# Kernel optimization log

Measured on AMD Instinct MI355X. Metric: run time of the kernel, lower is better.

Reference implementation:

```python
import jax, jax.numpy as jnp
import numpy as np
from jax import lax

B, M, L = 4, 20, 200
IN_C, C1, C2 = 2048, 512, 256
CDIM, DC1, DC2, SDIM = 300, 512, 256, 1024
NEG = -1e15  # -INFINITY in source


def conv1d(x, w, b, pad):
    # x: [N, Cin, L], w: [Cout, Cin, K]
    y = lax.conv_general_dilated(x, w, (1,), ((pad, pad),),
                                 dimension_numbers=('NCH', 'OIH', 'NCH'))
    return y + b[None, :, None]


def maxpool2(x):
    return lax.reduce_window(x, -jnp.inf, lax.max, (1, 1, 2), (1, 1, 2), 'VALID')


def deconv1d(x, w, b):
    # torch ConvTranspose1d(k=4, s=2, p=1): conv with lhs_dilation=2, pad k-1-p=2,
    # kernel flipped and in/out swapped. w: [Cin, Cout, K]
    wt = jnp.flip(w, -1).transpose(1, 0, 2)  # [Cout, Cin, K]
    y = lax.conv_general_dilated(x, wt, (1,), ((2, 2),), lhs_dilation=(2,),
                                 dimension_numbers=('NCH', 'OIH', 'NCH'))
    return y + b[None, :, None]


def setup_inputs() -> dict:
    key = jax.random.key(0)
    ks = jax.random.split(key, 16)
    p = lambda k, sh, s=0.02: (jax.random.normal(k, sh, jnp.float32) * s)
    return dict(
        batch=jax.random.normal(ks[0], (B, M, L, IN_C), jnp.float32),
        seg_len=jax.random.randint(ks[1], (B, M), 1, L + 1, jnp.int32),
        concept1=jax.random.normal(ks[2], (B, CDIM), jnp.float32),
        concept2=jax.random.normal(ks[3], (B, CDIM), jnp.float32),
        w_conv1=p(ks[4], (C1, IN_C, 5)), b_conv1=jnp.zeros((C1,), jnp.float32),
        w_conv2=p(ks[5], (C2, C1, 5)), b_conv2=jnp.zeros((C2,), jnp.float32),
        w_ca1=p(ks[6], (C2, CDIM)), w_ca2=p(ks[7], (C2, C2)), w_ca3=p(ks[8], (1, C2)),
        w_dc1=p(ks[9], (3 * C2, DC1, 4)), b_dc1=jnp.zeros((DC1,), jnp.float32),
        w_dc2=p(ks[10], (DC1, DC2, 4)), b_dc2=jnp.zeros((DC2,), jnp.float32),
        w_sim1=p(ks[11], (SDIM, DC2)), w_sim2=p(ks[12], (SDIM, CDIM)),
        w_mlp=p(ks[13], (1, SDIM)), b_mlp=jnp.zeros((1,), jnp.float32),
    )


def reference(batch, seg_len, concept1, concept2,
              w_conv1, b_conv1, w_conv2, b_conv2,
              w_ca1, w_ca2, w_ca3,
              w_dc1, b_dc1, w_dc2, b_dc2,
              w_sim1, w_sim2, w_mlp, b_mlp):
    Bs, Ms, Ls = batch.shape[:3]
    Lq = Ls // 4
    x = batch.reshape(Bs * Ms, Ls, -1).transpose(0, 2, 1)        # [BM, IN_C, L]
    t1 = maxpool2(conv1d(x, w_conv1, b_conv1, 2))                # [BM, C1, L/2]
    t2 = maxpool2(conv1d(t1, w_conv2, b_conv2, 2)).transpose(0, 2, 1)  # [BM, L/4, C2]

    # vectorized ragged mask: k < ceil(seg_len/4)
    mask = (jnp.arange(Lq)[None, None, :] < ((seg_len + 3) // 4)[:, :, None])
    mask = mask.reshape(Bs * Ms, Lq)

    kproj = t2 @ w_ca2.T                                         # [BM, Lq, C2]

    def concept_att(concept):
        # additive attention; scores are identical across the query-frame dim,
        # so compute one row and broadcast the weighted sum.
        q = concept @ w_ca1.T                                    # [B, C2]
        qe = jnp.repeat(q, Ms, axis=0)                           # [BM, C2]
        s = jnp.tanh(qe[:, None, :] + kproj) @ w_ca3[0]          # [BM, Lq]
        s = jnp.where(mask, s, NEG)
        a = jax.nn.softmax(s, axis=-1)
        r = jnp.einsum('bk,bkc->bc', a, t2)                      # [BM, C2]
        return jnp.broadcast_to(r[:, None, :], t2.shape)         # [BM, Lq, C2]

    r1 = concept_att(concept1)
    r2 = concept_att(concept2)

    cat = jnp.concatenate([t2, r1, r2], axis=-1).transpose(0, 2, 1)  # [BM, 3C2, Lq]
    d = deconv1d(cat, w_dc1, b_dc1)                              # [BM, DC1, L/2]
    d = deconv1d(d, w_dc2, b_dc2).transpose(0, 2, 1)             # [BM, L, DC2]
    d = d.reshape(Bs, Ms * Ls, -1)

    sim1 = d @ w_sim1.T                                          # [B, M*L, SDIM]
    c1 = concept1 @ w_sim2.T                                     # [B, SDIM]
    c2 = concept2 @ w_sim2.T
    sc1 = jax.nn.sigmoid((c1[:, None, :] * sim1) @ w_mlp[0] + b_mlp[0])
    sc2 = jax.nn.sigmoid((c2[:, None, :] * sim1) @ w_mlp[0] + b_mlp[0])
    return sc1.reshape(Bs, Ms, Ls), sc2.reshape(Bs, Ms, Ls)
```

## Files before the change

kernel.cpp:

```cpp
#include <hip/hip_runtime.h>
#include <hip/hip_bf16.h>
#include <math.h>

#define BB 4
#define MM 20
#define LL 200
#define INC 2048
#define C1 512
#define C2 256
#define CDIM 300
#define DC1 512
#define DC2 256
#define SDIM 1024
#define BM 80
#define L2 100
#define L4 50

typedef unsigned short u16;
typedef __attribute__((ext_vector_type(8))) short bf16x8;
typedef __attribute__((ext_vector_type(4))) float f32x4;

__device__ __forceinline__ u16 f2bf_rne(float f) {
  unsigned u = __float_as_uint(f);
  unsigned r = u + 0x7FFFu + ((u >> 16) & 1u);
  return (u16)(r >> 16);
}
__device__ __forceinline__ float bf2f(u16 v) {
  return __uint_as_float(((unsigned)v) << 16);
}

__device__ __forceinline__ void gload16(const u16* g, u16* l) {
  __builtin_amdgcn_global_load_lds(
      (const __attribute__((address_space(1))) void*)g,
      (__attribute__((address_space(3))) void*)l, 16, 0, 0);
}

__global__ void k_cast_pad_batch(const float* __restrict__ in, u16* __restrict__ out) {
  int idx = blockIdx.x * 256 + threadIdx.x;
  if (idx >= 80 * 204 * 256) return;
  int c8 = idx % 256;
  int pi = (idx / 256) % 204;
  int n  = idx / (256 * 204);
  uint4 o = make_uint4(0u, 0u, 0u, 0u);
  if (pi >= 2 && pi < 202) {
    const float* p = in + ((long long)(n * 200 + pi - 2) * 2048 + c8 * 8);
    float4 a = *(const float4*)p;
    float4 b = *(const float4*)(p + 4);
    o.x = (unsigned)f2bf_rne(a.x) | ((unsigned)f2bf_rne(a.y) << 16);
    o.y = (unsigned)f2bf_rne(a.z) | ((unsigned)f2bf_rne(a.w) << 16);
    o.z = (unsigned)f2bf_rne(b.x) | ((unsigned)f2bf_rne(b.y) << 16);
    o.w = (unsigned)f2bf_rne(b.z) | ((unsigned)f2bf_rne(b.w) << 16);
  }
  *(uint4*)(out + (long long)idx * 8) = o;
}

__global__ void k_zero_pad(u16* __restrict__ p, int ncnt, int rpad, int lr, int P,
                           int cin8, int total) {
  int idx = blockIdx.x * 256 + threadIdx.x;
  if (idx >= total) return;
  int c = idx % cin8;
  int pr = (idx / cin8) % (rpad - lr);
  int n = idx / (cin8 * (rpad - lr));
  int row = (pr < P) ? pr : lr + pr;
  *(uint4*)(p + ((long long)(n * rpad + row) * cin8 + c) * 8) = make_uint4(0, 0, 0, 0);
}

__global__ void k_cast_bf16(const float* __restrict__ in, u16* __restrict__ out, int n8) {
  int idx = blockIdx.x * 256 + threadIdx.x;
  if (idx >= n8) return;
  const float4* p = (const float4*)in + (long long)idx * 2;
  float4 a = p[0], b = p[1];
  uint4 o;
  o.x = (unsigned)f2bf_rne(a.x) | ((unsigned)f2bf_rne(a.y) << 16);
  o.y = (unsigned)f2bf_rne(a.z) | ((unsigned)f2bf_rne(a.w) << 16);
  o.z = (unsigned)f2bf_rne(b.x) | ((unsigned)f2bf_rne(b.y) << 16);
  o.w = (unsigned)f2bf_rne(b.z) | ((unsigned)f2bf_rne(b.w) << 16);
  *(uint4*)(out + (long long)idx * 8) = o;
}

__global__ void k_conv_w_t(const float* __restrict__ in, u16* __restrict__ out,
                           int Cout, int Cin, int Kk) {
  int idx = blockIdx.x * 256 + threadIdx.x;
  int total = Cout * Cin * Kk;
  if (idx >= total) return;
  int ci = idx % Cin;
  int t  = (idx / Cin) % Kk;
  int co = idx / (Cin * Kk);
  out[idx] = f2bf_rne(in[(co * Cin + ci) * Kk + t]);
}

__global__ void k_deconv_w_par(const float* __restrict__ in, u16* __restrict__ out,
                               int Cin, int Cout) {
  int idx = blockIdx.x * 256 + threadIdx.x;
  int total = Cin * Cout * 4;
  if (idx >= total) return;
  int ci = idx % Cin;
  int tt = (idx / Cin) & 1;
  int co = (idx / (2 * Cin)) % Cout;
  int zz = idx / (2 * Cin * Cout);
  out[idx] = f2bf_rne(in[(ci * Cout + co) * 4 + 3 - zz - 2 * tt]);
}

__global__ __launch_bounds__(256) void k_prep_small(
    const float* __restrict__ concept1, const float* __restrict__ concept2,
    const float* __restrict__ w_ca1, const float* __restrict__ w_sim1,
    const float* __restrict__ w_sim2, const float* __restrict__ w_mlp,
    float* __restrict__ qv) {
  int cz = blockIdx.x >> 2;
  int b  = blockIdx.x & 3;
  const float* con = cz ? concept2 : concept1;
  __shared__ float cvec[CDIM];
  __shared__ float chat[SDIM];
  int tid = threadIdx.x;
  for (int j = tid; j < CDIM; j += 256) cvec[j] = con[b * CDIM + j];
  __syncthreads();
  float accq = 0.f;
  for (int j = 0; j < CDIM; ++j) accq += cvec[j] * w_ca1[tid * CDIM + j];
  qv[(cz * 4 + b) * 256 + tid] = accq;
  for (int i = 0; i < 4; ++i) {
    int s = tid + i * 256;
    float a2 = 0.f;
    for (int j = 0; j < CDIM; ++j) a2 += cvec[j] * w_sim2[s * CDIM + j];
    chat[s] = a2 * w_mlp[s];
  }
  __syncthreads();
  float v = 0.f;
  for (int s = 0; s < SDIM; ++s) v += w_sim1[s * 256 + tid] * chat[s];
  qv[2048 + (cz * 4 + b) * 256 + tid] = v;
}

#define EP_PLAIN 0
#define EP_POOL  1
#define EP_ILV   2

template <int EP>
__global__ __launch_bounds__(256) void k_gemm(
    const u16* __restrict__ A, const u16* __restrict__ Bw,
    void* __restrict__ Co, const float* __restrict__ bias,
    int M, int N, int Ktot, int nchunk,
    int lr, int rpad, int cin, int off0c, int taps,
    int px, int yspan, int gy, long long sB, int orpad, int ooff) {
  __shared__ __align__(16) u16 As[2][8192];
  __shared__ __align__(16) u16 Bs[2][8192];
  int id = blockIdx.x;
  int k8 = id & 7, j = id >> 3;
  int x = k8 / px, h = k8 - x * px;
  int y = h * yspan + j;
  if (y >= gy) return;
  int z = blockIdx.z;
  int off0 = (EP == EP_ILV) ? z : off0c;
  int row0 = y * 128, col0 = x * 128;
  int tid = threadIdx.x, w = tid >> 6, ln = tid & 63;
  const u16* Bz = Bw + (long long)z * sB;

  const u16* ga[4];
  const u16* gb[4];
  #pragma unroll
  for (int i = 0; i < 4; ++i) {
    int f = 4 * w + i, blk = f >> 1, ks = f & 1;
    int klocal = ks * 32 + (ln >> 4) * 8;
    int ar = row0 + blk * 16 + (ln & 15);
    int n_ = ar / lr, l_ = ar - n_ * lr;
    ga[i] = A + ((long long)(n_ * rpad + l_ + off0) * cin + klocal);
    int br = col0 + blk * 16 + (ln & 15);
    gb[i] = Bz + ((long long)br * Ktot + klocal);
  }
  int wbase = 4 * w * 512;

  f32x4 acc[4][4];
  #pragma unroll
  for (int i = 0; i < 4; ++i)
    #pragma unroll
    for (int j2 = 0; j2 < 4; ++j2) acc[i][j2] = (f32x4){0.f, 0.f, 0.f, 0.f};

  int wr2 = (w >> 1) * 4;
  int wc2 = (w & 1) * 4;

  long long dstep = cin;
  long long dwrap = 64 - (long long)(taps - 1) * cin;
  int tc = 0;

  #pragma unroll
  for (int i = 0; i < 4; ++i) {
    gload16(ga[i], As[0] + wbase + i * 512);
    gload16(gb[i], Bs[0] + wbase + i * 512);
  }
  {
    long long d = (tc == taps - 1) ? dwrap : dstep;
    tc = (tc == taps - 1) ? 0 : tc + 1;
    #pragma unroll
    for (int i = 0; i < 4; ++i) { ga[i] += d; gb[i] += d; }
  }

  for (int c = 0; c < nchunk; ++c) {
    int cur = c & 1;
    if (c + 1 < nchunk) {
      u16* dA = As[cur ^ 1] + wbase;
      u16* dB = Bs[cur ^ 1] + wbase;
      #pragma unroll
      for (int i = 0; i < 4; ++i) {
        gload16(ga[i], dA + i * 512);
        gload16(gb[i], dB + i * 512);
      }
      long long d = (tc == taps - 1) ? dwrap : dstep;
      tc = (tc == taps - 1) ? 0 : tc + 1;
      #pragma unroll
      for (int i = 0; i < 4; ++i) { ga[i] += d; gb[i] += d; }
      asm volatile("s_waitcnt vmcnt(8)" ::: "memory");
    } else {
      asm volatile("s_waitcnt vmcnt(0)" ::: "memory");
    }
    __builtin_amdgcn_s_barrier();
    __builtin_amdgcn_sched_barrier(0);
    #pragma unroll
    for (int ks = 0; ks < 2; ++ks) {
      bf16x8 af[4], bf[4];
      #pragma unroll
      for (int mi = 0; mi < 4; ++mi)
        af[mi] = *(const bf16x8*)&As[cur][(((wr2 + mi) * 2 + ks) * 512) + ln * 8];
      #pragma unroll
      for (int ni = 0; ni < 4; ++ni)
        bf[ni] = *(const bf16x8*)&Bs[cur][(((wc2 + ni) * 2 + ks) * 512) + ln * 8];
      #pragma unroll
      for (int mi = 0; mi < 4; ++mi)
        #pragma unroll
        for (int ni = 0; ni < 4; ++ni)
          acc[mi][ni] = __builtin_amdgcn_mfma_f32_16x16x32_bf16(
              af[mi], bf[ni], acc[mi][ni], 0, 0, 0);
    }
    __builtin_amdgcn_sched_barrier(0);
    __builtin_amdgcn_s_barrier();
  }

  int c15 = ln & 15, q4 = (ln >> 4) * 4;
  int wrow = (w >> 1) * 64, wcol = (w & 1) * 64;
  if (EP == EP_PLAIN) {
    float* Cz = (float*)Co;
    #pragma unroll
    for (int mi = 0; mi < 4; ++mi) {
      int gbase = row0 + wrow + mi * 16 + q4;
      #pragma unroll
      for (int r = 0; r < 4; ++r) {
        int grow = gbase + r;
        if (grow < M) {
          #pragma unroll
          for (int ni = 0; ni < 4; ++ni) {
            int col = col0 + wcol + ni * 16 + c15;
            Cz[(long long)grow * N + col] = acc[mi][ni][r];
          }
        }
      }
    }
  } else if (EP == EP_POOL) {
    u16* Cz = (u16*)Co;
    int lrh = lr >> 1;
    #pragma unroll
    for (int mi = 0; mi < 4; ++mi) {
      int gbase = row0 + wrow + mi * 16 + q4;
      #pragma unroll
      for (int p = 0; p < 2; ++p) {
        int grow = gbase + 2 * p;
        if (grow < M) {
          int prow = grow >> 1;
          int n = prow / lrh, ll = prow - n * lrh;
          long long orow = (long long)n * orpad + ooff + ll;
          #pragma unroll
          for (int ni = 0; ni < 4; ++ni) {
            int col = col0 + wcol + ni * 16 + c15;
            float v = fmaxf(acc[mi][ni][2 * p], acc[mi][ni][2 * p + 1]) + bias[col];
            Cz[orow * N + col] = f2bf_rne(v);
          }
        }
      }
    }
  } else {
    u16* Cz = (u16*)Co;
    #pragma unroll
    for (int mi = 0; mi < 4; ++mi) {
      int gbase = row0 + wrow + mi * 16 + q4;
      #pragma unroll
      for (int r = 0; r < 4; ++r) {
        int grow = gbase + r;
        if (grow < M) {
          int n = grow / lr, l = grow - n * lr;
          long long orow = (long long)n * orpad + ooff + 2 * l + z;
          #pragma unroll
          for (int ni = 0; ni < 4; ++ni) {
            int col = col0 + wcol + ni * 16 + c15;
            Cz[orow * N + col] = f2bf_rne(acc[mi][ni][r] + bias[col]);
          }
        }
      }
    }
  }
}

__global__ __launch_bounds__(256) void k_attention(
    const float* __restrict__ kproj, const u16* __restrict__ t2b,
    const float* __restrict__ qv, const float* __restrict__ w_ca3,
    const int* __restrict__ seg_len, u16* __restrict__ rb) {
  int bm = blockIdx.x % BM;
  int cz = blockIdx.x / BM;
  int b = bm / MM;
  int tid = threadIdx.x, w = tid >> 6, ln = tid & 63;
  __shared__ float sq[256], sw[256], sa[L4 + 14];
  sq[tid] = qv[(cz * 4 + b) * 256 + tid];
  sw[tid] = w_ca3[tid];
  __syncthreads();
  int kmax = (seg_len[bm] + 3) >> 2;
  for (int k = w; k < L4; k += 4) {
    float val = 0.f;
    #pragma unroll
    for (int i = 0; i < 4; ++i) {
      int c = ln + 64 * i;
      val += tanhf(sq[c] + kproj[(bm * L4 + k) * 256 + c]) * sw[c];
    }
    for (int off = 32; off > 0; off >>= 1) val += __shfl_down(val, off, 64);
    if (ln == 0) sa[k] = (k < kmax) ? val : -1e15f;
  }
  __syncthreads();
  if (w == 0) {
    float sv = (ln < L4) ? sa[ln] : -3e38f;
    float mx = sv;
    for (int off = 32; off > 0; off >>= 1) mx = fmaxf(mx, __shfl_down(mx, off, 64));
    mx = __shfl(mx, 0, 64);
    float e = (ln < L4) ? expf(sv - mx) : 0.f;
    float s = e;
    for (int off = 32; off > 0; off >>= 1) s += __shfl_down(s, off, 64);
    s = __shfl(s, 0, 64);
    if (ln < L4) sa[ln] = e / s;
  }
  __syncthreads();
  float r = 0.f;
  for (int k = 0; k < L4; ++k) r += sa[k] * bf2f(t2b[(bm * L4 + k) * 256 + tid]);
  rb[(cz * BM + bm) * 256 + tid] = f2bf_rne(r);
}

__global__ void k_build_cat(const u16* __restrict__ t2b, const u16* __restrict__ rb,
                            u16* __restrict__ catm, int total) {
  int idx = blockIdx.x * 256 + threadIdx.x;
  if (idx >= total) return;
  int ci = idx % 768;
  int row = idx / 768;
  int bm = row / L4, li = row - bm * L4;
  u16 v;
  if (ci < 256)      v = t2b[row * 256 + ci];
  else if (ci < 512) v = rb[bm * 256 + (ci - 256)];
  else               v = rb[(BM + bm) * 256 + (ci - 512)];
  catm[((long long)(bm * 52 + 1 + li)) * 768 + ci] = v;
}

__global__ __launch_bounds__(256) void k_final(
    const u16* __restrict__ d2b, const float* __restrict__ qv,
    const float* __restrict__ b_mlp, float* __restrict__ out) {
  int row = blockIdx.x;
  int n = row / LL, lo = row % LL;
  int b = n / MM, m = n % MM;
  int tid = threadIdx.x;
  float v = bf2f(d2b[(long long)row * 256 + tid]);
  float p1 = v * qv[2048 + (0 * 4 + b) * 256 + tid];
  float p2 = v * qv[2048 + (1 * 4 + b) * 256 + tid];
  for (int off = 32; off > 0; off >>= 1) {
    p1 += __shfl_down(p1, off, 64);
    p2 += __shfl_down(p2, off, 64);
  }
  __shared__ float s1[4], s2[4];
  if ((tid & 63) == 0) { s1[tid >> 6] = p1; s2[tid >> 6] = p2; }
  __syncthreads();
  if (tid == 0) {
    float bmlp = b_mlp[0];
    float a1 = s1[0] + s1[1] + s1[2] + s1[3] + bmlp;
    float a2 = s2[0] + s2[1] + s2[2] + s2[3] + bmlp;
    int t_idx = m * LL + lo;
    out[b * 4000 + t_idx]         = 1.f / (1.f + expf(-a1));
    out[16000 + b * 4000 + t_idx] = 1.f / (1.f + expf(-a2));
  }
}

extern "C" void kernel_launch(void* const* d_in, const int* in_sizes, int n_in,
                              void* d_out, int out_size, void* d_ws, size_t ws_size,
                              hipStream_t stream) {
  const float* batch    = (const float*)d_in[0];
  const int*   seg_len  = (const int*)d_in[1];
  const float* concept1 = (const float*)d_in[2];
  const float* concept2 = (const float*)d_in[3];
  const float* w_conv1  = (const float*)d_in[4];
  const float* b_conv1  = (const float*)d_in[5];
  const float* w_conv2  = (const float*)d_in[6];
  const float* b_conv2  = (const float*)d_in[7];
  const float* w_ca1    = (const float*)d_in[8];
  const float* w_ca2    = (const float*)d_in[9];
  const float* w_ca3    = (const float*)d_in[10];
  const float* w_dc1    = (const float*)d_in[11];
  const float* b_dc1    = (const float*)d_in[12];
  const float* w_dc2    = (const float*)d_in[13];
  const float* b_dc2    = (const float*)d_in[14];
  const float* w_sim1   = (const float*)d_in[15];
  const float* w_sim2   = (const float*)d_in[16];
  const float* w_mlp    = (const float*)d_in[17];
  const float* b_mlp    = (const float*)d_in[18];
  float* out = (float*)d_out;

  float* ws = (float*)d_ws;
  const long long off_qv    = 0;
  const long long off_kproj = 4096;
  const long long off_rb    = 1028096;
  const long long off_t1    = 1048576;
  const long long off_t2    = 3211264;
  const long long off_w1b   = 3735552;
  const long long off_w2b   = 6356992;
  const long long off_wd1p  = 6684672;
  const long long off_wd2p  = 7471104;
  const long long off_wca2b = 7733248;
  const long long off_BIG   = 7766016;

  u16* rb    = (u16*)(ws + off_rb);
  u16* t1b   = (u16*)(ws + off_t1);
  u16* t2b   = (u16*)(ws + off_t2);
  u16* w1b   = (u16*)(ws + off_w1b);
  u16* w2b   = (u16*)(ws + off_w2b);
  u16* wd1p  = (u16*)(ws + off_wd1p);
  u16* wd2p  = (u16*)(ws + off_wd2p);
  u16* wca2b = (u16*)(ws + off_wca2b);
  u16* batchb = (u16*)(ws + off_BIG);
  u16* catm   = (u16*)(ws + off_BIG);
  u16* d1b    = (u16*)(ws + off_BIG) + 3342336;
  u16* d2b    = (u16*)(ws + off_BIG) + 7667712;

  k_cast_pad_batch<<<dim3(16320), 256, 0, stream>>>(batch, batchb);
  k_conv_w_t<<<dim3(20480), 256, 0, stream>>>(w_conv1, w1b, C1, INC, 5);
  k_conv_w_t<<<dim3(2560), 256, 0, stream>>>(w_conv2, w2b, C2, C1, 5);
  k_deconv_w_par<<<dim3(6144), 256, 0, stream>>>(w_dc1, wd1p, 3 * C2, DC1);
  k_deconv_w_par<<<dim3(2048), 256, 0, stream>>>(w_dc2, wd2p, DC1, DC2);
  k_cast_bf16<<<dim3(32), 256, 0, stream>>>(w_ca2, wca2b, 8192);
  k_prep_small<<<dim3(8), 256, 0, stream>>>(concept1, concept2, w_ca1, w_sim1, w_sim2,
                                            w_mlp, ws + off_qv);
  k_zero_pad<<<dim3(80), 256, 0, stream>>>(t1b, 80, 104, 100, 2, 64, 20480);

  k_gemm<EP_POOL><<<dim3(504), 256, 0, stream>>>(
      batchb, w1b, t1b, b_conv1, 16000, 512, 10240, 160,
      200, 204, 2048, 0, 5, 2, 63, 125, 0, 104, 2);

  k_zero_pad<<<dim3(60), 256, 0, stream>>>(catm, 80, 52, 50, 1, 96, 15360);
  k_zero_pad<<<dim3(40), 256, 0, stream>>>(d1b, 80, 102, 100, 1, 64, 10240);

  k_gemm<EP_POOL><<<dim3(128), 256, 0, stream>>>(
      t1b, w2b, t2b, b_conv2, 8000, 256, 2560, 40,
      100, 104, 512, 0, 5, 4, 16, 63, 0, 50, 0);

  k_gemm<EP_PLAIN><<<dim3(64), 256, 0, stream>>>(
      t2b, wca2b, ws + off_kproj, nullptr, 4000, 256, 256, 4,
      4000, 4000, 256, 0, 1, 4, 8, 32, 0, 0, 0);

  k_attention<<<dim3(160), 256, 0, stream>>>(ws + off_kproj, t2b, ws + off_qv,
                                             w_ca3, seg_len, rb);

  k_build_cat<<<dim3(12000), 256, 0, stream>>>(t2b, rb, catm, 4000 * 768);

  k_gemm<EP_ILV><<<dim3(128, 1, 2), 256, 0, stream>>>(
      catm, wd1p, d1b, b_dc1, 4000, 512, 1536, 24,
      50, 52, 768, 0, 2, 2, 16, 32, 786432LL, 102, 1);

  k_gemm<EP_ILV><<<dim3(128, 1, 2), 256, 0, stream>>>(
      d1b, wd2p, d2b, b_dc2, 8000, 256, 1024, 16,
      100, 102, 512, 0, 2, 4, 16, 63, 262144LL, 200, 0);

  k_final<<<dim3(16000), 256, 0, stream>>>(d2b, ws + off_qv, b_mlp, out);
}
```

Measured before the change: 874.5 us.

## Add tap-reusing conv GEMM with XOR-swizzled input layout for both convolutions

Adds a dedicated convolution GEMM kernel that stages one 132-row input slab per 64-channel block into shared memory and reuses it across all 5 kernel taps by shifting row offsets, instead of reloading A for each tap. The padded batch buffer and the conv1 output are written in an XOR-swizzled 16-byte-chunk layout so the shifted-row LDS reads avoid bank conflicts. The aim is to cut global and LDS traffic for the A operand in conv1 and conv2. In exchange it uses a larger shared-memory footprint and hand-tuned waitcnt counts, and it ties the producers and consumers to a matching swizzle convention.

```diff
diff --git a/kernel.cpp b/kernel.cpp
--- a/kernel.cpp
+++ b/kernel.cpp
@@ -51,7 +51,9 @@
     o.z = (unsigned)f2bf_rne(b.x) | ((unsigned)f2bf_rne(b.y) << 16);
     o.w = (unsigned)f2bf_rne(b.z) | ((unsigned)f2bf_rne(b.w) << 16);
   }
-  *(uint4*)(out + (long long)idx * 8) = o;
+  int key = (n * 204 + pi) & 7;
+  long long pos = ((long long)(n * 204 + pi)) * 256 + (c8 ^ key);
+  *(uint4*)(out + pos * 8) = o;
 }
 
 __global__ void k_zero_pad(u16* __restrict__ p, int ncnt, int rpad, int lr, int P,
@@ -127,6 +129,147 @@
   float v = 0.f;
   for (int s = 0; s < SDIM; ++s) v += w_sim1[s * 256 + tid] * chat[s];
   qv[2048 + (cz * 4 + b) * 256 + tid] = v;
+}
+
+template <int SWZO>
+__global__ __launch_bounds__(256) void k_gemm_conv(
+    const u16* __restrict__ A, const u16* __restrict__ Bw,
+    u16* __restrict__ Co, const float* __restrict__ bias,
+    int M, int N, int Ktot, int cin, int ncib,
+    int lr, int rpad, int px, int yspan, int gy,
+    int orpad, int ooff, long long aend) {
+  __shared__ __align__(16) u16 At[2][10240];
+  __shared__ __align__(16) u16 Bs[2][8192];
+  int id = blockIdx.x;
+  int k8 = id & 7, j = id >> 3;
+  int x = k8 / px, h = k8 - x * px;
+  int y = h * yspan + j;
+  if (y >= gy) return;
+  int row0 = y * 128, col0 = x * 128;
+  int tid = threadIdx.x, w = tid >> 6, ln = tid & 63;
+  int r15 = ln & 15, q = ln >> 4;
+
+  int n0 = row0 / lr, l0 = row0 - n0 * lr;
+  long long prow0 = (long long)n0 * rpad + l0;
+
+  int wrb = (w >> 1) * 64;
+  int rlb[4], pp[4];
+  #pragma unroll
+  for (int mi = 0; mi < 4; ++mi) {
+    int rr = wrb + mi * 16 + r15;
+    int nc = (row0 + rr) / lr - n0;
+    rlb[mi] = rr + 4 * nc;
+    pp[mi] = (int)((prow0 + rlb[mi]) & 7);
+  }
+
+  long long arow_base = prow0 + w * 40 + (ln >> 3);
+  const u16* alim = A + (aend - 8);
+  auto stA = [&](int cib_, int pc) {
+    const u16* src = A + (arow_base + pc * 8) * cin + cib_ * 64 + (ln & 7) * 8;
+    if (src > alim) src = alim;
+    gload16(src, At[cib_ & 1] + (w * 40 + pc * 8) * 64);
+  };
+
+  const u16* gb[4];
+  #pragma unroll
+  for (int i = 0; i < 4; ++i) {
+    int f = 4 * w + i, blk = f >> 1, ks = f & 1;
+    int klocal = ks * 32 + q * 8;
+    int br = col0 + blk * 16 + r15;
+    gb[i] = Bw + ((long long)br * Ktot + klocal);
+  }
+  int wbase = 4 * w * 512;
+
+  f32x4 acc[4][4];
+  #pragma unroll
+  for (int i = 0; i < 4; ++i)
+    #pragma unroll
+    for (int j2 = 0; j2 < 4; ++j2) acc[i][j2] = (f32x4){0.f, 0.f, 0.f, 0.f};
+  int wc2 = (w & 1) * 4;
+
+  #pragma unroll
+  for (int pc = 0; pc < 5; ++pc) stA(0, pc);
+  #pragma unroll
+  for (int i = 0; i < 4; ++i) gload16(gb[i], Bs[0] + wbase + i * 512);
+  #pragma unroll
+  for (int i = 0; i < 4; ++i) gb[i] += cin;
+  int ts = 1;
+  asm volatile("s_waitcnt vmcnt(0)" ::: "memory");
+  __builtin_amdgcn_s_barrier();
+
+  long long bwrap = 64 - 4 * (long long)cin;
+  for (int cib = 0; cib < ncib; ++cib) {
+    bool lastcib = (cib == ncib - 1);
+    #pragma unroll
+    for (int t = 0; t < 5; ++t) {
+      bool lastc = lastcib && (t == 4);
+      if (!lastcib) stA(cib + 1, t);
+      if (!lastc) {
+        int bufn = (cib + t + 1) & 1;
+        #pragma unroll
+        for (int i = 0; i < 4; ++i) gload16(gb[i], Bs[bufn] + wbase + i * 512);
+        long long d = (ts == 4) ? bwrap : (long long)cin;
+        ts = (ts == 4) ? 0 : ts + 1;
+        #pragma unroll
+        for (int i = 0; i < 4; ++i) gb[i] += d;
+      }
+      if (lastc)        asm volatile("s_waitcnt vmcnt(0)" ::: "memory");
+      else if (lastcib) asm volatile("s_waitcnt vmcnt(4)" ::: "memory");
+      else              asm volatile("s_waitcnt vmcnt(5)" ::: "memory");
+      __builtin_amdgcn_s_barrier();
+      __builtin_amdgcn_sched_barrier(0);
+      const u16* Ab = At[cib & 1];
+      const u16* Bb = Bs[(cib + t) & 1];
+      int rof[4], pr8[4];
+      #pragma unroll
+      for (int mi = 0; mi < 4; ++mi) {
+        rof[mi] = (rlb[mi] + t) * 64;
+        pr8[mi] = (pp[mi] + t) & 7;
+      }
+      #pragma unroll
+      for (int ks = 0; ks < 2; ++ks) {
+        bf16x8 af[4], bf[4];
+        #pragma unroll
+        for (int mi = 0; mi < 4; ++mi)
+          af[mi] = *(const bf16x8*)&Ab[rof[mi] + (((ks * 4 + q) ^ pr8[mi]) * 8)];
+        #pragma unroll
+        for (int ni = 0; ni < 4; ++ni)
+          bf[ni] = *(const bf16x8*)&Bb[(((wc2 + ni) * 2 + ks) * 512) + ln * 8];
+        #pragma unroll
+        for (int mi = 0; mi < 4; ++mi)
+          #pragma unroll
+          for (int ni = 0; ni < 4; ++ni)
+            acc[mi][ni] = __builtin_amdgcn_mfma_f32_16x16x32_bf16(
+                af[mi], bf[ni], acc[mi][ni], 0, 0, 0);
+      }
+      __builtin_amdgcn_sched_barrier(0);
+      __builtin_amdgcn_s_barrier();
+    }
+  }
+
+  int q4 = q * 4;
+  int wrow = (w >> 1) * 64, wcol = (w & 1) * 64;
+  int lrh = lr >> 1;
+  #pragma unroll
+  for (int mi = 0; mi < 4; ++mi) {
+    int gbase = row0 + wrow + mi * 16 + q4;
+    #pragma unroll
+    for (int p = 0; p < 2; ++p) {
+      int grow = gbase + 2 * p;
+      if (grow < M) {
+        int prow = grow >> 1;
+        int n = prow / lrh, ll = prow - n * lrh;
+        long long orow = (long long)n * orpad + ooff + ll;
+        int key = SWZO ? ((int)(orow & 7) << 3) : 0;
+        #pragma unroll
+        for (int ni = 0; ni < 4; ++ni) {
+          int col = col0 + wcol + ni * 16 + r15;
+          float v = fmaxf(acc[mi][ni][2 * p], acc[mi][ni][2 * p + 1]) + bias[col];
+          Co[orow * N + (col ^ key)] = f2bf_rne(v);
+        }
+      }
+    }
+  }
 }
 
 #define EP_PLAIN 0
@@ -437,16 +580,16 @@
                                             w_mlp, ws + off_qv);
   k_zero_pad<<<dim3(80), 256, 0, stream>>>(t1b, 80, 104, 100, 2, 64, 20480);
 
-  k_gemm<EP_POOL><<<dim3(504), 256, 0, stream>>>(
-      batchb, w1b, t1b, b_conv1, 16000, 512, 10240, 160,
-      200, 204, 2048, 0, 5, 2, 63, 125, 0, 104, 2);
+  k_gemm_conv<1><<<dim3(504), 256, 0, stream>>>(
+      batchb, w1b, t1b, b_conv1, 16000, 512, 10240, 2048, 32,
+      200, 204, 2, 63, 125, 104, 2, 80LL * 204 * 2048);
 
   k_zero_pad<<<dim3(60), 256, 0, stream>>>(catm, 80, 52, 50, 1, 96, 15360);
   k_zero_pad<<<dim3(40), 256, 0, stream>>>(d1b, 80, 102, 100, 1, 64, 10240);
 
-  k_gemm<EP_POOL><<<dim3(128), 256, 0, stream>>>(
-      t1b, w2b, t2b, b_conv2, 8000, 256, 2560, 40,
-      100, 104, 512, 0, 5, 4, 16, 63, 0, 50, 0);
+  k_gemm_conv<0><<<dim3(128), 256, 0, stream>>>(
+      t1b, w2b, t2b, b_conv2, 8000, 256, 2560, 512, 8,
+      100, 104, 4, 16, 63, 50, 0, 80LL * 104 * 512);
 
   k_gemm<EP_PLAIN><<<dim3(64), 256, 0, stream>>>(
       t2b, wca2b, ws + off_kproj, nullptr, 4000, 256, 256, 4,
```

Result: faster. 749.8 us (-14.3%).
